# Kernel optimization log

Hardware: AMD Instinct MI355X
Metric: run time of the kernel (lower is better)

The kernel has to match this reference:

```python
import jax, jax.numpy as jnp
import numpy as np

M_FIELDS = 26   # cin_size[0]
H1 = 128        # cin_size[1]
H2 = 128        # cin_size[2]
BATCH = 2048
EMB_K = 32


def setup_inputs() -> dict:
    key = jax.random.key(0)
    k0, k1, k2, k3, k4 = jax.random.split(key, 5)
    inputs = jax.random.normal(k0, (BATCH, M_FIELDS, EMB_K), dtype=jnp.float32)
    # Conv3d(1, H1, kernel=(26,26,1)) -> weight [H1, H_prev=26, m=26], bias [H1]
    W1 = jax.random.normal(k1, (H1, M_FIELDS, M_FIELDS), dtype=jnp.float32) * 0.05
    b1 = jax.random.normal(k2, (H1,), dtype=jnp.float32) * 0.05
    # Conv3d(1, H2, kernel=(H1,26,1)) -> weight [H2, H1, m=26], bias [H2]
    W2 = jax.random.normal(k3, (H2, H1, M_FIELDS), dtype=jnp.float32) * 0.05
    b2 = jax.random.normal(k4, (H2,), dtype=jnp.float32) * 0.05
    return {"inputs": inputs, "W1": W1, "b1": b1, "W2": W2, "b2": b2}


def _cin_layer(x_prev, x0, W, b):
    # x_prev: [B, H_prev, k], x0: [B, m, k], W: [H, H_prev, m], b: [H]
    # Equivalent to: outer product z[b,i,j,k] = x_prev[b,i,k]*x0[b,j,k],
    # then Conv3d with kernel (H_prev, m, 1): out[b,h,k] = sum_ij W[h,i,j]*z + b[h]
    return jnp.einsum('bik,bjk,hij->bhk', x_prev, x0, W) + b[None, :, None]


def reference(inputs, W1, b1, W2, b2):
    x1 = _cin_layer(inputs, inputs, W1, b1)   # [B, H1, k]
    x2 = _cin_layer(x1, inputs, W2, b2)       # [B, H2, k]
    res = jnp.concatenate([x1, x2], axis=1)   # [B, H1+H2, k]
    return jnp.sum(res, axis=-1)              # [B, H1+H2]
```

## Files before the change

### kernel.cpp

```cpp
#include <hip/hip_runtime.h>

typedef __bf16 bf16;
typedef __bf16 bf16x8 __attribute__((ext_vector_type(8)));
typedef __bf16 bf16x4 __attribute__((ext_vector_type(4)));
typedef float f32x4 __attribute__((ext_vector_type(4)));
typedef unsigned int u32;

#define NB    2048
#define NM    26
#define NJP   27

__global__ __launch_bounds__(256) void prep_all(
    const float* __restrict__ W1, const float* __restrict__ W2,
    bf16* __restrict__ w1t, bf16* __restrict__ w2t2)
{
  const int bid = blockIdx.x, t = threadIdx.x;
  #pragma unroll
  for (int g = 0; g < 4; ++g) {
    int ge = g*160768 + bid*256 + t;
    if (ge < 110592) {
      int e = ge;
      int el = e & 7, lr = (e >> 3) & 15, lq = (e >> 7) & 3, ni = (e >> 9) & 3;
      int rest = e >> 11;
      int c = rest % NJP, cs_idx = rest / NJP;
      int h = cs_idx*64 + ni*16 + lr;
      int i = lq*8 + el;
      float v = (i < NM && c < NM) ? W1[h*(NM*NM) + i*NM + c] : 0.f;
      w1t[e] = (bf16)v;
    } else {
      int e = ge - 110592;
      int el = e & 7, lr = (e >> 3) & 15, lq = (e >> 7) & 3, ni = (e >> 9) & 3;
      int rest = e >> 11;
      int kc = rest % 130, cs_idx = rest / 130;
      int h = cs_idx*64 + ni*16 + lr;
      int c = lq*8 + el;
      float v = (kc < 128 && c < NM) ? W2[h*(128*NM) + kc*NM + c] : 0.f;
      w2t2[e] = (bf16)v;
    }
  }
}

#define STEP(CUR, NXT, J) do {                                                 \
  { int jn = ((J)+1 > 25) ? 25 : (J)+1;         \
    scf[NXT][0][0] = spw0[jn*32];  scf[NXT][0][1] = spw0[jn*32 + 16];          \
    scf[NXT][1][0] = spw1[jn*32];  scf[NXT][1][1] = spw1[jn*32 + 16]; }        \
  _Pragma("unroll")                                                            \
  for (int ni = 0; ni < 4; ++ni)                                               \
    B[NXT][ni] = *(const bf16x8*)(tb + (long)((J)+1)*2048 + ni*512);           \
  _Pragma("unroll")                                                            \
  for (int bb = 0; bb < 2; ++bb)                                               \
    _Pragma("unroll")                                                          \
    for (int mi = 0; mi < 2; ++mi) {                                           \
      bf16x8 af;                                                               \
      _Pragma("unroll")                                                        \
      for (int e = 0; e < 8; ++e)                                              \
        af[e] = (bf16)(xf32[bb][mi][e] * scf[CUR][bb][mi]);                    \
      _Pragma("unroll")                                                        \
      for (int ni = 0; ni < 4; ++ni)                                           \
        acc[bb][mi][ni] = __builtin_amdgcn_mfma_f32_16x16x32_bf16(af,          \
                                    B[CUR][ni], acc[bb][mi][ni], 0, 0, 0);     \
    }                                                                          \
} while (0)

#define STEPM(CUR, NXT, KL) do {                                               \
  Af[NXT] = *(const bf16x8*)&ldsG[(((KL)+1)*4 + lq)*72 + lr*8];                \
  Bf[NXT][0] = *(const bf16x8*)(Bb0 + (long)((KL)+1)*2048);                    \
  Bf[NXT][1] = *(const bf16x8*)(Bb1 + (long)((KL)+1)*2048);                    \
  _Pragma("unroll")                                                            \
  for (int ht = 0; ht < 2; ++ht)                                               \
    acc2[ht] = __builtin_amdgcn_mfma_f32_16x16x32_bf16(Af[CUR], Bf[CUR][ht],   \
                                                       acc2[ht], 0, 0, 0);     \
} while (0)

__global__ __launch_bounds__(256, 2) void cinfuse(
    const float* __restrict__ in, const bf16* __restrict__ w1t,
    const bf16* __restrict__ w2t2, const float* __restrict__ b1,
    const float* __restrict__ b2, float* __restrict__ out)
{
  __shared__ __align__(16) bf16 ldsT[4][64*36];
  __shared__ __align__(16) bf16 ldsG[264*72];
  const int t = threadIdx.x, bid = blockIdx.x;
  const int lane = t & 63, w = t >> 6;
  const int lr = lane & 15, lq = lane >> 4;
  const int fo = lq*128 + lr*8;
  const int cs_idx = bid & 1, cs = cs_idx * 64;
  const int grp = bid >> 1;
  const int bw0 = grp*8 + w*2;

  const float* bin0 = in + (long)bw0*(NM*32);
  const float* bin1 = bin0 + NM*32;
  const float* spw0 = bin0 + lr;
  const float* spw1 = bin1 + lr;

  float xf32[2][2][8];
  #pragma unroll
  for (int bb = 0; bb < 2; ++bb) {
    const float* bin = bb ? bin1 : bin0;
    #pragma unroll
    for (int mi = 0; mi < 2; ++mi)
      #pragma unroll
      for (int e = 0; e < 8; ++e) {
        int j = lq*8 + e;
        xf32[bb][mi][e] = (j < NM) ? bin[j*32 + mi*16 + lr] : 0.f;
      }
  }

  f32x4 acc[2][2][4];
  #pragma unroll
  for (int bb=0; bb<2; ++bb)
    #pragma unroll
    for (int mi=0; mi<2; ++mi)
      #pragma unroll
      for (int ni=0; ni<4; ++ni) acc[bb][mi][ni] = {0.f,0.f,0.f,0.f};

  const bf16* tb = w1t + (long)cs_idx*NJP*2048 + fo;

  float scf[2][2][2];
  bf16x8 B[2][4];
  #pragma unroll
  for (int ni = 0; ni < 4; ++ni)
    B[0][ni] = *(const bf16x8*)(tb + ni*512);
  scf[0][0][0] = spw0[0];  scf[0][0][1] = spw0[16];
  scf[0][1][0] = spw1[0];  scf[0][1][1] = spw1[16];

  for (int jj = 0; jj < 13; ++jj) {
    STEP(0, 1, 2*jj);
    STEP(1, 0, 2*jj + 1);
  }

  float bias[4];
  #pragma unroll
  for (int ni=0; ni<4; ++ni) bias[ni] = b1[cs + ni*16 + lr];

  bf16* T = &ldsT[w][0];

  #pragma unroll
  for (int bb = 0; bb < 2; ++bb) {
    const int bw = bw0 + bb;
    const int bloc = w*2 + bb;
    const float* bin = bb ? bin1 : bin0;

    #pragma unroll
    for (int ni=0; ni<4; ++ni) {
      float vv = 0.f;
      #pragma unroll
      for (int mi=0; mi<2; ++mi)
        #pragma unroll
        for (int r=0; r<4; ++r) vv += acc[bb][mi][ni][r];
      vv += __shfl_xor(vv, 16, 64);
      vv += __shfl_xor(vv, 32, 64);
      if (lq == 0) out[bw*256 + cs + ni*16 + lr] = vv + 32.0f * bias[ni];
    }

    #pragma unroll
    for (int mi=0; mi<2; ++mi)
      #pragma unroll
      for (int ni=0; ni<4; ++ni) {
        bf16x4 pk;
        #pragma unroll
        for (int r=0; r<4; ++r) pk[r] = (bf16)(acc[bb][mi][ni][r] + bias[ni]);
        *(bf16x4*)&T[(ni*16+lr)*36 + mi*16 + lq*4] = pk;
      }

    bf16x8 bg[2];
    #pragma unroll
    for (int nt = 0; nt < 2; ++nt) {
      int j = nt*16 + lr;
      bf16x8 vv;
      #pragma unroll
      for (int e=0; e<8; ++e) vv[e] = (bf16)0.f;
      if (j < NM) {
        const float* src = bin + j*32 + lq*8;
        f32x4 a = *(const f32x4*)src, c = *(const f32x4*)(src+4);
        #pragma unroll
        for (int e=0; e<4; ++e) { vv[e] = (bf16)a[e]; vv[4+e] = (bf16)c[e]; }
      }
      bg[nt] = vv;
    }
    #pragma unroll
    for (int mt = 0; mt < 4; ++mt) {
      bf16x8 ag = *(const bf16x8*)&T[(mt*16+lr)*36 + lq*8];
      #pragma unroll
      for (int nt = 0; nt < 2; ++nt) {
        f32x4 z = {0.f,0.f,0.f,0.f};
        f32x4 g = __builtin_amdgcn_mfma_f32_16x16x32_bf16(bg[nt], ag, z, 0, 0, 0);
        bf16x4 pk;
        #pragma unroll
        for (int r = 0; r < 4; ++r) pk[r] = (bf16)g[r];
        const int kh = (mt*16 + lr)*4 + nt*2 + (lq >> 1);
        *(bf16x4*)&ldsG[kh*72 + bloc*8 + (lq & 1)*4] = pk;
      }
    }
  }

  __syncthreads();

  const int ht0 = w*2, ht1 = w*2 + 1;
  const bf16* Bb0 = w2t2 + ((long)(ht0 >> 2)*130 + cs)*2048 + (ht0 & 3)*512 + fo;
  const bf16* Bb1 = w2t2 + ((long)(ht1 >> 2)*130 + cs)*2048 + (ht1 & 3)*512 + fo;

  f32x4 acc2[2];
  acc2[0] = {0.f,0.f,0.f,0.f};  acc2[1] = {0.f,0.f,0.f,0.f};

  bf16x8 Af[2], Bf[2][2];
  Af[0] = *(const bf16x8*)&ldsG[lq*72 + lr*8];
  Bf[0][0] = *(const bf16x8*)Bb0;
  Bf[0][1] = *(const bf16x8*)Bb1;

  for (int jj = 0; jj < 32; ++jj) {
    STEPM(0, 1, 2*jj);
    STEPM(1, 0, 2*jj + 1);
  }

  if (cs_idx == 0) {
    #pragma unroll
    for (int ht = 0; ht < 2; ++ht) {
      float bv = 32.0f * b2[(w*2 + ht)*16 + lr];
      #pragma unroll
      for (int r=0; r<4; ++r) acc2[ht][r] += bv;
    }
  }

  if (lq < 2) {
    #pragma unroll
    for (int ht = 0; ht < 2; ++ht) {
      int h = (w*2 + ht)*16 + lr;
      #pragma unroll
      for (int r=0; r<4; ++r) {
        int b = grp*8 + lq*4 + r;
        atomicAdd(&out[b*256 + 128 + h], acc2[ht][r]);
      }
    }
  }
}

extern "C" void kernel_launch(void* const* d_in, const int* in_sizes, int n_in,
                              void* d_out, int out_size, void* d_ws, size_t ws_size,
                              hipStream_t stream) {
  const float* in = (const float*)d_in[0];
  const float* W1 = (const float*)d_in[1];
  const float* b1 = (const float*)d_in[2];
  const float* W2 = (const float*)d_in[3];
  const float* b2 = (const float*)d_in[4];
  float* out = (float*)d_out;

  char* ws = (char*)d_ws;
  bf16* w1t  = (bf16*)(ws);
  bf16* w2t2 = (bf16*)(ws + 1048576);

  prep_all<<<628, 256, 0, stream>>>(W1, W2, w1t, w2t2);
  cinfuse <<<512, 256, 0, stream>>>(in, w1t, w2t2, b1, b2, out);
}
```

Measured before the change: 95.19 us.

## Alias transpose scratch into G buffer, deepen W2 prefetch, raise occupancy to 3

The per-wave transpose scratch now lives inside the G LDS buffer instead of a separate array. The operands are pulled into registers and a barrier is added before G is written, which shrinks the LDS footprint. Launch bounds request 3 blocks per CU instead of 2, and the layer-2 loop prefetches W2 fragments three steps ahead with a 4-deep register ring instead of one step. The extra registers (agr, bgr, deeper Bf) may cause spills under the tighter register budget from the higher occupancy target, and the added barrier adds a sync.

```diff
diff --git a/kernel.cpp b/kernel.cpp
--- a/kernel.cpp
+++ b/kernel.cpp
@@ -62,23 +62,22 @@
     }                                                                          \
 } while (0)
 
-#define STEPM(CUR, NXT, KL) do {                                               \
-  Af[NXT] = *(const bf16x8*)&ldsG[(((KL)+1)*4 + lq)*72 + lr*8];                \
-  Bf[NXT][0] = *(const bf16x8*)(Bb0 + (long)((KL)+1)*2048);                    \
-  Bf[NXT][1] = *(const bf16x8*)(Bb1 + (long)((KL)+1)*2048);                    \
+#define STEPM(CA, NA, KL, Q) do {                                              \
+  Af[NA] = *(const bf16x8*)&ldsU[(((KL)+1)*4 + lq)*72 + lr*8];                 \
+  Bf[((Q)+3)&3][0] = *(const bf16x8*)(Bb0 + (long)((KL)+3)*2048);              \
+  Bf[((Q)+3)&3][1] = *(const bf16x8*)(Bb1 + (long)((KL)+3)*2048);              \
   _Pragma("unroll")                                                            \
   for (int ht = 0; ht < 2; ++ht)                                               \
-    acc2[ht] = __builtin_amdgcn_mfma_f32_16x16x32_bf16(Af[CUR], Bf[CUR][ht],   \
+    acc2[ht] = __builtin_amdgcn_mfma_f32_16x16x32_bf16(Af[CA], Bf[(Q)][ht],    \
                                                        acc2[ht], 0, 0, 0);     \
 } while (0)
 
-__global__ __launch_bounds__(256, 2) void cinfuse(
+__global__ __launch_bounds__(256, 3) void cinfuse(
     const float* __restrict__ in, const bf16* __restrict__ w1t,
     const bf16* __restrict__ w2t2, const float* __restrict__ b1,
     const float* __restrict__ b2, float* __restrict__ out)
 {
-  __shared__ __align__(16) bf16 ldsT[4][64*36];
-  __shared__ __align__(16) bf16 ldsG[264*72];
+  __shared__ __align__(16) bf16 ldsU[264*72];
   const int t = threadIdx.x, bid = blockIdx.x;
   const int lane = t & 63, w = t >> 6;
   const int lr = lane & 15, lq = lane >> 4;
@@ -132,12 +131,14 @@
   #pragma unroll
   for (int ni=0; ni<4; ++ni) bias[ni] = b1[cs + ni*16 + lr];
 
-  bf16* T = &ldsT[w][0];
+  bf16* T = &ldsU[w*2304];
+
+  bf16x8 agr[2][4];
+  bf16x8 bgr[2][2];
 
   #pragma unroll
   for (int bb = 0; bb < 2; ++bb) {
     const int bw = bw0 + bb;
-    const int bloc = w*2 + bb;
     const float* bin = bb ? bin1 : bin0;
 
     #pragma unroll
@@ -162,7 +163,10 @@
         *(bf16x4*)&T[(ni*16+lr)*36 + mi*16 + lq*4] = pk;
       }
 
-    bf16x8 bg[2];
+    #pragma unroll
+    for (int mt = 0; mt < 4; ++mt)
+      agr[bb][mt] = *(const bf16x8*)&T[(mt*16+lr)*36 + lq*8];
+
     #pragma unroll
     for (int nt = 0; nt < 2; ++nt) {
       int j = nt*16 + lr;
@@ -175,20 +179,27 @@
         #pragma unroll
         for (int e=0; e<4; ++e) { vv[e] = (bf16)a[e]; vv[4+e] = (bf16)c[e]; }
       }
-      bg[nt] = vv;
-    }
+      bgr[bb][nt] = vv;
+    }
+  }
+
+  __syncthreads();
+
+  #pragma unroll
+  for (int bb = 0; bb < 2; ++bb) {
+    const int bloc = w*2 + bb;
     #pragma unroll
     for (int mt = 0; mt < 4; ++mt) {
-      bf16x8 ag = *(const bf16x8*)&T[(mt*16+lr)*36 + lq*8];
       #pragma unroll
       for (int nt = 0; nt < 2; ++nt) {
         f32x4 z = {0.f,0.f,0.f,0.f};
-        f32x4 g = __builtin_amdgcn_mfma_f32_16x16x32_bf16(bg[nt], ag, z, 0, 0, 0);
+        f32x4 g = __builtin_amdgcn_mfma_f32_16x16x32_bf16(bgr[bb][nt],
+                                                          agr[bb][mt], z, 0, 0, 0);
         bf16x4 pk;
         #pragma unroll
         for (int r = 0; r < 4; ++r) pk[r] = (bf16)g[r];
         const int kh = (mt*16 + lr)*4 + nt*2 + (lq >> 1);
-        *(bf16x4*)&ldsG[kh*72 + bloc*8 + (lq & 1)*4] = pk;
+        *(bf16x4*)&ldsU[kh*72 + bloc*8 + (lq & 1)*4] = pk;
       }
     }
   }
@@ -202,14 +213,20 @@
   f32x4 acc2[2];
   acc2[0] = {0.f,0.f,0.f,0.f};  acc2[1] = {0.f,0.f,0.f,0.f};
 
-  bf16x8 Af[2], Bf[2][2];
-  Af[0] = *(const bf16x8*)&ldsG[lq*72 + lr*8];
-  Bf[0][0] = *(const bf16x8*)Bb0;
-  Bf[0][1] = *(const bf16x8*)Bb1;
-
-  for (int jj = 0; jj < 32; ++jj) {
-    STEPM(0, 1, 2*jj);
-    STEPM(1, 0, 2*jj + 1);
+  bf16x8 Af[2], Bf[4][2];
+  Af[0] = *(const bf16x8*)&ldsU[lq*72 + lr*8];
+  #pragma unroll
+  for (int d = 0; d < 3; ++d) {
+    Bf[d][0] = *(const bf16x8*)(Bb0 + (long)d*2048);
+    Bf[d][1] = *(const bf16x8*)(Bb1 + (long)d*2048);
+  }
+
+  for (int jj = 0; jj < 16; ++jj) {
+    const int KL0 = jj*4;
+    STEPM(0, 1, KL0+0, 0);
+    STEPM(1, 0, KL0+1, 1);
+    STEPM(0, 1, KL0+2, 2);
+    STEPM(1, 0, KL0+3, 3);
   }
 
   if (cs_idx == 0) {
```

Result: faster. 92.57 us, median of 2 (-2.8%).
